# Kernel optimization log

Hardware: AMD Instinct MI355X
Metric: run time of the kernel (lower is better)

## Reference

```python
import jax, jax.numpy as jnp
import numpy as np

K, N = 4096, 4096
GROUP_SIZE = 64
N_GROUPS = N // GROUP_SIZE
B, S = 4, 2048
NBITS = 4


def setup_inputs() -> dict:
    key = jax.random.key(0)
    ks = jax.random.split(key, 7)
    x = jax.random.normal(ks[0], (B, S, N), dtype=jnp.float32)
    # per-group scales/zeros broadcast over the group_size axis
    scales = jax.random.uniform(ks[1], (K, N_GROUPS, 1), dtype=jnp.float32, minval=0.001, maxval=0.05)
    zeros = jax.random.uniform(ks[2], (K, N_GROUPS, 1), dtype=jnp.float32, minval=0.0, maxval=2.0 ** NBITS - 1)
    mu1 = jax.random.uniform(ks[3], (N,), dtype=jnp.float32, minval=0.5, maxval=1.5)
    mu2 = jax.random.uniform(ks[4], (K,), dtype=jnp.float32, minval=0.5, maxval=1.5)
    bias = jax.random.normal(ks[5], (K,), dtype=jnp.float32)
    W_q = jax.random.randint(ks[6], (K, N), 0, 2 ** NBITS, dtype=jnp.int32)
    return {"x": x, "scales": scales, "zeros": zeros, "mu1": mu1, "mu2": mu2, "bias": bias, "W_q": W_q}


def reference(x, scales, zeros, mu1, mu2, bias, W_q):
    # dequantize: per-group (Q - zero) * scale, then Sinkhorn rescale mu2 (rows) * mu1 (cols)
    k, n = W_q.shape
    n_groups = scales.shape[1]
    Qg = W_q.astype(jnp.float32).reshape(k, n_groups, -1)  # [K, G, gs]
    W_deq = ((Qg - zeros) * scales).reshape(k, n) * mu2[:, None] * mu1[None, :]
    W_deq = W_deq.astype(x.dtype)
    # nn.functional.linear: x @ W^T + b
    return jnp.einsum('bsn,kn->bsk', x, W_deq) + bias
```

## Files before the change

kernel.cpp:

```cpp
#include <hip/hip_runtime.h>
#include <hip/hip_bf16.h>
#include <stdint.h>
#include <type_traits>

typedef unsigned short u16;
typedef __bf16 bf16x8 __attribute__((ext_vector_type(8)));
typedef float f32x4 __attribute__((ext_vector_type(4)));

#define M_TOT 8192
#define N_TOT 4096
#define K_TOT 4096
#define BM 256
#define BN 256
#define BK 64
#define NT 64

#define HALF_EL 8192
#define B_OFF   16384
#define SLOT_EL 32768
#define SLOT_BYTES 65536

template <int V> using ic = std::integral_constant<int, V>;
template <bool V> using bc = std::integral_constant<bool, V>;

__device__ __forceinline__ u16 f2bf(float f) {
    union { float f; uint32_t u; } v; v.f = f;
    uint32_t u = v.u;
    return (u16)((u + 0x7fffu + ((u >> 16) & 1u)) >> 16);
}

__global__ __launch_bounds__(256) void cvt_x_kernel(const float* __restrict__ x,
                                                    u16* __restrict__ xb) {
    const int i = blockIdx.x * blockDim.x + threadIdx.x;
    const float4* p = (const float4*)x + (size_t)i * 2;
    float4 v0 = p[0], v1 = p[1];
    uint4 o;
    o.x = (uint32_t)f2bf(v0.x) | ((uint32_t)f2bf(v0.y) << 16);
    o.y = (uint32_t)f2bf(v0.z) | ((uint32_t)f2bf(v0.w) << 16);
    o.z = (uint32_t)f2bf(v1.x) | ((uint32_t)f2bf(v1.y) << 16);
    o.w = (uint32_t)f2bf(v1.z) | ((uint32_t)f2bf(v1.w) << 16);
    *((uint4*)(xb + (size_t)i * 8)) = o;
}

__global__ __launch_bounds__(256) void deq_w_kernel(const int* __restrict__ wq,
                                                    const float* __restrict__ scales,
                                                    const float* __restrict__ zeros,
                                                    const float* __restrict__ mu1,
                                                    const float* __restrict__ mu2,
                                                    u16* __restrict__ wb) {
    const int i = blockIdx.x * blockDim.x + threadIdx.x;
    const int k  = i >> 9;
    const int n0 = (i & 511) << 3;
    const int g  = n0 >> 6;
    const float z  = zeros[k * 64 + g];
    const float sm = scales[k * 64 + g] * mu2[k];
    const int4* qp = (const int4*)(wq + (size_t)k * N_TOT + n0);
    int4 q0 = qp[0], q1 = qp[1];
    const float4* mp = (const float4*)(mu1 + n0);
    float4 u0 = mp[0], u1 = mp[1];
    uint4 o;
    o.x = (uint32_t)f2bf(((float)q0.x - z) * sm * u0.x) |
          ((uint32_t)f2bf(((float)q0.y - z) * sm * u0.y) << 16);
    o.y = (uint32_t)f2bf(((float)q0.z - z) * sm * u0.z) |
          ((uint32_t)f2bf(((float)q0.w - z) * sm * u0.w) << 16);
    o.z = (uint32_t)f2bf(((float)q1.x - z) * sm * u1.x) |
          ((uint32_t)f2bf(((float)q1.y - z) * sm * u1.y) << 16);
    o.w = (uint32_t)f2bf(((float)q1.z - z) * sm * u1.z) |
          ((uint32_t)f2bf(((float)q1.w - z) * sm * u1.w) << 16);
    *((uint4*)(wb + (size_t)k * N_TOT + n0)) = o;
}

__global__ __launch_bounds__(512, 2) void gemm_kernel(const u16* __restrict__ Xb,
                                                      const u16* __restrict__ Wb,
                                                      const float* __restrict__ bias,
                                                      float* __restrict__ out) {
    __shared__ __align__(16) u16 lds[2 * SLOT_EL];

    const int bid = blockIdx.x;
    const int cpx = gridDim.x >> 3;
    const int swz = (bid & 7) * cpx + (bid >> 3);
    const int bm = swz >> 4;
    const int bn = swz & 15;

    const int tid  = threadIdx.x;
    const int w    = tid >> 6;
    const int lane = tid & 63;
    const int wm = w >> 2, wn = w & 3;

    const int scol = (((lane & 7) ^ (lane >> 3)) << 3);
    const u16* aT = Xb + (size_t)(bm * BM + w * 16 + (lane >> 3)) * N_TOT + scol;
    const u16* bT = Wb + (size_t)(bn * BN + w * 16 + (lane >> 3)) * N_TOT + scol;

    u16* const sdA = &lds[w * 1024];
    u16* const sdB = &lds[B_OFF + w * 1024];

    auto gload = [](const u16* s, u16* d) {
        __builtin_amdgcn_global_load_lds(
            (const __attribute__((address_space(1))) uint32_t*)s,
            (__attribute__((address_space(3))) uint32_t*)d, 16, 0, 0);
    };
    auto stA = [&](auto SlC, auto Hc, auto Dc) {
        const u16* s = aT + (size_t)(Hc.value * 128) * N_TOT + Dc.value;
        u16* d = sdA + SlC.value * SLOT_EL + Hc.value * HALF_EL;
        gload(s, d); gload(s + (size_t)8 * N_TOT, d + 512);
    };
    auto stB = [&](auto SlC, auto Hc, auto Dc) {
        const u16* s = bT + (size_t)(Hc.value * 128) * N_TOT + Dc.value;
        u16* d = sdB + SlC.value * SLOT_EL + Hc.value * HALF_EL;
        gload(s, d); gload(s + (size_t)8 * N_TOT, d + 512);
    };

    const int cc0 = (((lane >> 4) << 3)) ^ ((lane & 7) << 3);
    const int rA  = ((wm << 4) + (lane & 15)) << 6;
    const int rB  = ((wn << 4) + (lane & 15)) << 6;
    int oAa = (rA + cc0) * 2;
    int oAb = (rA + (cc0 ^ 32)) * 2;
    int oBa = (B_OFF + rB + cc0) * 2;
    int oBb = (B_OFF + rB + (cc0 ^ 32)) * 2;
    const char* const ldsc = (const char*)lds;

    f32x4 acc[2][2][4][2] = {};
    bf16x8 afLo[4][2], afHi[4][2];
    bf16x8 bf0[2][2], bf1[2][2];

    auto rd_afLo_next = [&]() {
        const int xa = oAa ^ SLOT_BYTES, xb2 = oAb ^ SLOT_BYTES;
        #pragma unroll
        for (int j = 0; j < 4; ++j) {
            afLo[j][0] = *(const bf16x8*)(ldsc + xa + j * 4096);
            afLo[j][1] = *(const bf16x8*)(ldsc + xb2 + j * 4096);
        }
    };
    auto rd_bf0_next = [&]() {
        const int xa = oBa ^ SLOT_BYTES, xb2 = oBb ^ SLOT_BYTES;
        #pragma unroll
        for (int j2 = 0; j2 < 2; ++j2) {
            bf0[j2][0] = *(const bf16x8*)(ldsc + xa + j2 * 8192);
            bf0[j2][1] = *(const bf16x8*)(ldsc + xb2 + j2 * 8192);
        }
    };
    auto rd_afHi_cur = [&]() {
        #pragma unroll
        for (int j = 0; j < 4; ++j) {
            afHi[j][0] = *(const bf16x8*)(ldsc + oAa + 16384 + j * 4096);
            afHi[j][1] = *(const bf16x8*)(ldsc + oAb + 16384 + j * 4096);
        }
    };
    auto rd_bf1_cur = [&]() {
        #pragma unroll
        for (int j2 = 0; j2 < 2; ++j2) {
            bf1[j2][0] = *(const bf16x8*)(ldsc + oBa + 16384 + j2 * 8192);
            bf1[j2][1] = *(const bf16x8*)(ldsc + oBb + 16384 + j2 * 8192);
        }
    };

    #define MFMA_CLUSTER(A, B, MH, NH)                                          \
        __builtin_amdgcn_s_setprio(1);                                          \
        _Pragma("unroll")                                                       \
        for (int ks = 0; ks < 2; ++ks)                                          \
            _Pragma("unroll")                                                   \
            for (int j = 0; j < 4; ++j)                                         \
                _Pragma("unroll")                                               \
                for (int j2 = 0; j2 < 2; ++j2)                                  \
                    acc[MH][NH][j][j2] = __builtin_amdgcn_mfma_f32_16x16x32_bf16(\
                        A[j][ks], B[j2][ks], acc[MH][NH][j][j2], 0, 0, 0);      \
        __builtin_amdgcn_s_setprio(0);

    auto ktile = [&](auto SlC, auto St0, auto St2, auto RdN,
                     auto V1c, auto V3c, auto D0, auto D1) {
        constexpr int SL = SlC.value;
        rd_bf1_cur();
        if constexpr (St0.value) { stA(ic<SL ^ 1>{}, ic<1>{}, D0);
                                   stB(ic<SL ^ 1>{}, ic<1>{}, D0); }
        MFMA_CLUSTER(afLo, bf0, 0, 0)
        rd_afHi_cur();
        MFMA_CLUSTER(afLo, bf1, 0, 1)
        if constexpr (V1c.value == 4) asm volatile("s_waitcnt vmcnt(4)" ::: "memory");
        else if constexpr (V1c.value == 0) asm volatile("s_waitcnt vmcnt(0)" ::: "memory");
        __builtin_amdgcn_s_barrier();
        __builtin_amdgcn_sched_barrier(0);
        if constexpr (RdN.value) rd_afLo_next();
        if constexpr (St2.value) { stA(SlC, ic<0>{}, D1);
                                   stB(SlC, ic<0>{}, D1); }
        MFMA_CLUSTER(afHi, bf1, 1, 1)
        MFMA_CLUSTER(afHi, bf0, 1, 0)
        if constexpr (RdN.value) rd_bf0_next();
        if constexpr (V3c.value == 4) asm volatile("s_waitcnt vmcnt(4)" ::: "memory");
        else if constexpr (V3c.value == 0) asm volatile("s_waitcnt vmcnt(0)" ::: "memory");
        __builtin_amdgcn_s_barrier();
        __builtin_amdgcn_sched_barrier(0);
        oAa ^= SLOT_BYTES; oAb ^= SLOT_BYTES; oBa ^= SLOT_BYTES; oBb ^= SLOT_BYTES;
    };

    stA(ic<0>{}, ic<0>{}, ic<0>{});  stB(ic<0>{}, ic<0>{}, ic<0>{});
    stA(ic<0>{}, ic<1>{}, ic<0>{});  stB(ic<0>{}, ic<1>{}, ic<0>{});
    stA(ic<1>{}, ic<0>{}, ic<BK>{}); stB(ic<1>{}, ic<0>{}, ic<BK>{});
    asm volatile("s_waitcnt vmcnt(4)" ::: "memory");
    __builtin_amdgcn_s_barrier();
    __builtin_amdgcn_sched_barrier(0);
    {
        #pragma unroll
        for (int j = 0; j < 4; ++j) {
            afLo[j][0] = *(const bf16x8*)(ldsc + oAa + j * 4096);
            afLo[j][1] = *(const bf16x8*)(ldsc + oAb + j * 4096);
        }
        #pragma unroll
        for (int j2 = 0; j2 < 2; ++j2) {
            bf0[j2][0] = *(const bf16x8*)(ldsc + oBa + j2 * 8192);
            bf0[j2][1] = *(const bf16x8*)(ldsc + oBb + j2 * 8192);
        }
    }

    for (int it = 0; it < 31; ++it) {
        ktile(ic<0>{}, bc<true>{}, bc<true>{}, bc<true>{},
              ic<4>{}, ic<4>{}, ic<BK>{}, ic<2 * BK>{});
        ktile(ic<1>{}, bc<true>{}, bc<true>{}, bc<true>{},
              ic<4>{}, ic<4>{}, ic<2 * BK>{}, ic<3 * BK>{});
        aT += 2 * BK;
        bT += 2 * BK;
    }
    ktile(ic<0>{}, bc<true>{}, bc<false>{}, bc<true>{},
          ic<4>{}, ic<0>{}, ic<BK>{}, ic<0>{});
    ktile(ic<1>{}, bc<false>{}, bc<false>{}, bc<false>{},
          ic<-1>{}, ic<-1>{}, ic<0>{}, ic<0>{});

    #undef MFMA_CLUSTER

    #pragma unroll
    for (int mh_ = 0; mh_ < 2; ++mh_)
        #pragma unroll
        for (int j = 0; j < 4; ++j)
            #pragma unroll
            for (int rr = 0; rr < 4; ++rr) {
                const int row = bm * BM + mh_ * 128 + j * 32 + wm * 16 + ((lane >> 4) << 2) + rr;
                float* orow = out + (size_t)row * K_TOT;
                #pragma unroll
                for (int nh_ = 0; nh_ < 2; ++nh_)
                    #pragma unroll
                    for (int j2 = 0; j2 < 2; ++j2) {
                        const int col = bn * BN + nh_ * 128 + j2 * 64 + wn * 16 + (lane & 15);
                        orow[col] = acc[mh_][nh_][j][j2][rr] + bias[col];
                    }
            }
}

extern "C" void kernel_launch(void* const* d_in, const int* in_sizes, int n_in,
                              void* d_out, int out_size, void* d_ws, size_t ws_size,
                              hipStream_t stream) {
    const float* x      = (const float*)d_in[0];
    const float* scales = (const float*)d_in[1];
    const float* zeros  = (const float*)d_in[2];
    const float* mu1    = (const float*)d_in[3];
    const float* mu2    = (const float*)d_in[4];
    const float* bias   = (const float*)d_in[5];
    const int*   wq     = (const int*)d_in[6];
    float* out = (float*)d_out;

    u16* xb = (u16*)d_ws;
    u16* wb = (u16*)d_ws + (size_t)M_TOT * N_TOT;

    cvt_x_kernel<<<(M_TOT * N_TOT / 8) / 256, 256, 0, stream>>>(x, xb);
    deq_w_kernel<<<(K_TOT * N_TOT / 8) / 256, 256, 0, stream>>>(wq, scales, zeros, mu1, mu2, wb);
    gemm_kernel<<<(M_TOT / BM) * (K_TOT / BN), 512, 0, stream>>>(xb, wb, bias, out);
}
```

Before: 265.5 us.

## Merge prep kernels into one launch and add intra-ktile barriers in GEMM

Combines the x-to-bf16 conversion and weight dequantization into a single prep kernel launch, split by block index, removing one kernel launch and the serialization between the two passes. In the GEMM k-tile loop it inserts extra s_barrier calls between each MFMA cluster and the LDS reads, and drops the sched_barrier fences, so waves stay in lockstep and the compiler has more freedom to schedule. The extra barriers add sync overhead and could reduce overlap between waves, while removing the sched_barrier calls may let the compiler reorder LDS and MFMA work in unintended ways.

Result: slower. 277.5 us (+4.5%).

```diff
diff --git a/kernel.cpp b/kernel.cpp
--- a/kernel.cpp
+++ b/kernel.cpp
@@ -20,6 +20,9 @@
 #define SLOT_EL 32768
 #define SLOT_BYTES 65536
 
+#define CVT_BLOCKS 16384
+#define DEQ_BLOCKS 8192
+
 template <int V> using ic = std::integral_constant<int, V>;
 template <bool V> using bc = std::integral_constant<bool, V>;
 
@@ -29,45 +32,47 @@
     return (u16)((u + 0x7fffu + ((u >> 16) & 1u)) >> 16);
 }
 
-__global__ __launch_bounds__(256) void cvt_x_kernel(const float* __restrict__ x,
-                                                    u16* __restrict__ xb) {
-    const int i = blockIdx.x * blockDim.x + threadIdx.x;
-    const float4* p = (const float4*)x + (size_t)i * 2;
-    float4 v0 = p[0], v1 = p[1];
-    uint4 o;
-    o.x = (uint32_t)f2bf(v0.x) | ((uint32_t)f2bf(v0.y) << 16);
-    o.y = (uint32_t)f2bf(v0.z) | ((uint32_t)f2bf(v0.w) << 16);
-    o.z = (uint32_t)f2bf(v1.x) | ((uint32_t)f2bf(v1.y) << 16);
-    o.w = (uint32_t)f2bf(v1.z) | ((uint32_t)f2bf(v1.w) << 16);
-    *((uint4*)(xb + (size_t)i * 8)) = o;
-}
-
-__global__ __launch_bounds__(256) void deq_w_kernel(const int* __restrict__ wq,
-                                                    const float* __restrict__ scales,
-                                                    const float* __restrict__ zeros,
-                                                    const float* __restrict__ mu1,
-                                                    const float* __restrict__ mu2,
-                                                    u16* __restrict__ wb) {
-    const int i = blockIdx.x * blockDim.x + threadIdx.x;
-    const int k  = i >> 9;
-    const int n0 = (i & 511) << 3;
-    const int g  = n0 >> 6;
-    const float z  = zeros[k * 64 + g];
-    const float sm = scales[k * 64 + g] * mu2[k];
-    const int4* qp = (const int4*)(wq + (size_t)k * N_TOT + n0);
-    int4 q0 = qp[0], q1 = qp[1];
-    const float4* mp = (const float4*)(mu1 + n0);
-    float4 u0 = mp[0], u1 = mp[1];
-    uint4 o;
-    o.x = (uint32_t)f2bf(((float)q0.x - z) * sm * u0.x) |
-          ((uint32_t)f2bf(((float)q0.y - z) * sm * u0.y) << 16);
-    o.y = (uint32_t)f2bf(((float)q0.z - z) * sm * u0.z) |
-          ((uint32_t)f2bf(((float)q0.w - z) * sm * u0.w) << 16);
-    o.z = (uint32_t)f2bf(((float)q1.x - z) * sm * u1.x) |
-          ((uint32_t)f2bf(((float)q1.y - z) * sm * u1.y) << 16);
-    o.w = (uint32_t)f2bf(((float)q1.z - z) * sm * u1.z) |
-          ((uint32_t)f2bf(((float)q1.w - z) * sm * u1.w) << 16);
-    *((uint4*)(wb + (size_t)k * N_TOT + n0)) = o;
+__global__ __launch_bounds__(256) void prep_kernel(const float* __restrict__ x,
+                                                   u16* __restrict__ xb,
+                                                   const int* __restrict__ wq,
+                                                   const float* __restrict__ scales,
+                                                   const float* __restrict__ zeros,
+                                                   const float* __restrict__ mu1,
+                                                   const float* __restrict__ mu2,
+                                                   u16* __restrict__ wb) {
+    const int b = blockIdx.x;
+    if (b < CVT_BLOCKS) {
+        const int i = b * 256 + threadIdx.x;
+        const float4* p = (const float4*)x + (size_t)i * 2;
+        float4 v0 = p[0], v1 = p[1];
+        uint4 o;
+        o.x = (uint32_t)f2bf(v0.x) | ((uint32_t)f2bf(v0.y) << 16);
+        o.y = (uint32_t)f2bf(v0.z) | ((uint32_t)f2bf(v0.w) << 16);
+        o.z = (uint32_t)f2bf(v1.x) | ((uint32_t)f2bf(v1.y) << 16);
+        o.w = (uint32_t)f2bf(v1.z) | ((uint32_t)f2bf(v1.w) << 16);
+        *((uint4*)(xb + (size_t)i * 8)) = o;
+    } else {
+        const int i = (b - CVT_BLOCKS) * 256 + threadIdx.x;
+        const int k  = i >> 9;
+        const int n0 = (i & 511) << 3;
+        const int g  = n0 >> 6;
+        const float z  = zeros[k * 64 + g];
+        const float sm = scales[k * 64 + g] * mu2[k];
+        const int4* qp = (const int4*)(wq + (size_t)k * N_TOT + n0);
+        int4 q0 = qp[0], q1 = qp[1];
+        const float4* mp = (const float4*)(mu1 + n0);
+        float4 u0 = mp[0], u1 = mp[1];
+        uint4 o;
+        o.x = (uint32_t)f2bf(((float)q0.x - z) * sm * u0.x) |
+              ((uint32_t)f2bf(((float)q0.y - z) * sm * u0.y) << 16);
+        o.y = (uint32_t)f2bf(((float)q0.z - z) * sm * u0.z) |
+              ((uint32_t)f2bf(((float)q0.w - z) * sm * u0.w) << 16);
+        o.z = (uint32_t)f2bf(((float)q1.x - z) * sm * u1.x) |
+              ((uint32_t)f2bf(((float)q1.y - z) * sm * u1.y) << 16);
+        o.w = (uint32_t)f2bf(((float)q1.z - z) * sm * u1.z) |
+              ((uint32_t)f2bf(((float)q1.w - z) * sm * u1.w) << 16);
+        *((uint4*)(wb + (size_t)k * N_TOT + n0)) = o;
+    }
 }
 
 __global__ __launch_bounds__(512, 2) void gemm_kernel(const u16* __restrict__ Xb,
@@ -166,29 +171,35 @@
                         A[j][ks], B[j2][ks], acc[MH][NH][j][j2], 0, 0, 0);      \
         __builtin_amdgcn_s_setprio(0);
 
+    auto vmw = [](auto Vc) {
+        if constexpr (Vc.value == 4) asm volatile("s_waitcnt vmcnt(4)" ::: "memory");
+        else if constexpr (Vc.value == 0) asm volatile("s_waitcnt vmcnt(0)" ::: "memory");
+    };
+
     auto ktile = [&](auto SlC, auto St0, auto St2, auto RdN,
                      auto V1c, auto V3c, auto D0, auto D1) {
         constexpr int SL = SlC.value;
         rd_bf1_cur();
         if constexpr (St0.value) { stA(ic<SL ^ 1>{}, ic<1>{}, D0);
                                    stB(ic<SL ^ 1>{}, ic<1>{}, D0); }
+        __builtin_amdgcn_s_barrier();
         MFMA_CLUSTER(afLo, bf0, 0, 0)
+        __builtin_amdgcn_s_barrier();
         rd_afHi_cur();
+        __builtin_amdgcn_s_barrier();
         MFMA_CLUSTER(afLo, bf1, 0, 1)
-        if constexpr (V1c.value == 4) asm volatile("s_waitcnt vmcnt(4)" ::: "memory");
-        else if constexpr (V1c.value == 0) asm volatile("s_waitcnt vmcnt(0)" ::: "memory");
-        __builtin_amdgcn_s_barrier();
-        __builtin_amdgcn_sched_barrier(0);
+        vmw(V1c);
+        __builtin_amdgcn_s_barrier();
         if constexpr (RdN.value) rd_afLo_next();
         if constexpr (St2.value) { stA(SlC, ic<0>{}, D1);
                                    stB(SlC, ic<0>{}, D1); }
+        __builtin_amdgcn_s_barrier();
         MFMA_CLUSTER(afHi, bf1, 1, 1)
+        __builtin_amdgcn_s_barrier();
         MFMA_CLUSTER(afHi, bf0, 1, 0)
         if constexpr (RdN.value) rd_bf0_next();
-        if constexpr (V3c.value == 4) asm volatile("s_waitcnt vmcnt(4)" ::: "memory");
-        else if constexpr (V3c.value == 0) asm volatile("s_waitcnt vmcnt(0)" ::: "memory");
-        __builtin_amdgcn_s_barrier();
-        __builtin_amdgcn_sched_barrier(0);
+        vmw(V3c);
+        __builtin_amdgcn_s_barrier();
         oAa ^= SLOT_BYTES; oAb ^= SLOT_BYTES; oBa ^= SLOT_BYTES; oBb ^= SLOT_BYTES;
     };
 
@@ -197,7 +208,6 @@
     stA(ic<1>{}, ic<0>{}, ic<BK>{}); stB(ic<1>{}, ic<0>{}, ic<BK>{});
     asm volatile("s_waitcnt vmcnt(4)" ::: "memory");
     __builtin_amdgcn_s_barrier();
-    __builtin_amdgcn_sched_barrier(0);
     {
         #pragma unroll
         for (int j = 0; j < 4; ++j) {
@@ -259,7 +269,7 @@
     u16* xb = (u16*)d_ws;
     u16* wb = (u16*)d_ws + (size_t)M_TOT * N_TOT;
 
-    cvt_x_kernel<<<(M_TOT * N_TOT / 8) / 256, 256, 0, stream>>>(x, xb);
-    deq_w_kernel<<<(K_TOT * N_TOT / 8) / 256, 256, 0, stream>>>(wq, scales, zeros, mu1, mu2, wb);
+    prep_kernel<<<CVT_BLOCKS + DEQ_BLOCKS, 256, 0, stream>>>(
+        x, xb, wq, scales, zeros, mu1, mu2, wb);
     gemm_kernel<<<(M_TOT / BM) * (K_TOT / BN), 512, 0, stream>>>(xb, wb, bias, out);
 }
```
